# Kernel optimization log

Measured on AMD Instinct MI355X. Metric: run time of the kernel, lower is better.

Reference implementation:

```python
import jax, jax.numpy as jnp
import numpy as np

HIDDEN, HEADS, KV_HEADS, HEAD_DIM = 2048, 8, 1, 256
B, L = 2, 4096
ROPE_BASE = 10000.0


def _rope_tables(seq_len, dim, offset=0):
    inv_freq = 1.0 / (ROPE_BASE ** (jnp.arange(0, dim, 2, dtype=jnp.float32) / dim))
    t = jnp.arange(offset, offset + seq_len, dtype=jnp.float32)
    freqs = jnp.einsum('l,d->ld', t, inv_freq)          # [L, dim/2]
    emb = jnp.concatenate([freqs, freqs], axis=-1)      # [L, dim]
    return jnp.cos(emb), jnp.sin(emb)


def _rotate_half(x):
    x1, x2 = jnp.split(x, 2, axis=-1)
    return jnp.concatenate([-x2, x1], axis=-1)


def _apply_rope(x, cos, sin):
    # x: [B, H, L, D]; cos/sin: [L, D] broadcast over B, H
    return x * cos + _rotate_half(x) * sin


def setup_inputs() -> dict:
    key = jax.random.key(0)
    ks = jax.random.split(key, 5)
    s = lambda fan_in: 1.0 / np.sqrt(fan_in)
    return {
        'x':   jax.random.normal(ks[0], (B, L, HIDDEN), jnp.float32),
        'q_w': jax.random.normal(ks[1], (HEADS * HEAD_DIM, HIDDEN), jnp.float32) * s(HIDDEN),
        'k_w': jax.random.normal(ks[2], (KV_HEADS * HEAD_DIM, HIDDEN), jnp.float32) * s(HIDDEN),
        'v_w': jax.random.normal(ks[3], (KV_HEADS * HEAD_DIM, HIDDEN), jnp.float32) * s(HIDDEN),
        'o_w': jax.random.normal(ks[4], (HIDDEN, HEADS * HEAD_DIM), jnp.float32) * s(HEADS * HEAD_DIM),
    }


def reference(x, q_w, k_w, v_w, o_w):
    b, l, _ = x.shape
    g = HEADS // KV_HEADS  # kv groups
    # projections (nn.Linear: x @ W^T)
    q = (x @ q_w.T).reshape(b, l, HEADS, HEAD_DIM).transpose(0, 2, 1, 3)      # [B,H,L,D]
    k = (x @ k_w.T).reshape(b, l, KV_HEADS, HEAD_DIM).transpose(0, 2, 1, 3)   # [B,Hk,L,D]
    v = (x @ v_w.T).reshape(b, l, KV_HEADS, HEAD_DIM).transpose(0, 2, 1, 3)
    cos, sin = _rope_tables(l, HEAD_DIM, offset=0)
    q = _apply_rope(q, cos, sin)
    k = _apply_rope(k, cos, sin)
    # GQA attention without materializing repeated KV heads
    qg = q.reshape(b, KV_HEADS, g, l, HEAD_DIM)
    scale = HEAD_DIM ** -0.5
    scores = jnp.einsum('bkgqd,bkld->bkgql', qg, k) * scale                   # [B,Hk,g,L,L]
    attn = jax.nn.softmax(scores.astype(jnp.float32), axis=-1).astype(q.dtype)
    out = jnp.einsum('bkgql,bkld->bkgqd', attn, v)                            # [B,Hk,g,L,D]
    out = out.reshape(b, HEADS, l, HEAD_DIM).transpose(0, 2, 1, 3).reshape(b, l, HEADS * HEAD_DIM)
    return out @ o_w.T
```

## Files before the change

kernel.cpp:

```cpp
#include <hip/hip_runtime.h>
#include <cstdint>

typedef __bf16 bf16x8 __attribute__((ext_vector_type(8)));
typedef float f32x4 __attribute__((ext_vector_type(4)));
typedef float f32x16 __attribute__((ext_vector_type(16)));
typedef short s16x4 __attribute__((ext_vector_type(4)));
typedef int i32x4 __attribute__((ext_vector_type(4)));

static __device__ __forceinline__ short bf_bits(float f) {
  uint32_t u = __builtin_bit_cast(uint32_t, f);
  u += 0x7fffu + ((u >> 16) & 1u);
  return (short)(u >> 16);
}
static __device__ __forceinline__ float bf_f(short s) {
  uint32_t u = ((uint32_t)(uint16_t)s) << 16;
  return __builtin_bit_cast(float, u);
}
static __device__ __forceinline__ bf16x8 ld_frag(const short* p) {
  i32x4 v = *reinterpret_cast<const i32x4*>(p);
  return __builtin_bit_cast(bf16x8, v);
}

typedef __attribute__((address_space(3))) uint32_t lds_u32_t;
typedef const __attribute__((address_space(1))) uint32_t glb_u32_t;
static __device__ __forceinline__ void gl_lds16(const void* g, const void* l) {
  __builtin_amdgcn_global_load_lds((glb_u32_t*)g,
                                   (lds_u32_t*)(uint32_t)(uintptr_t)l,
                                   16, 0, 0);
}

__global__ void cvt_bf16(const float* __restrict__ in, short* __restrict__ out, int n4) {
  int i = blockIdx.x * blockDim.x + threadIdx.x;
  if (i >= n4) return;
  float4 v = reinterpret_cast<const float4*>(in)[i];
  s16x4 o = { bf_bits(v.x), bf_bits(v.y), bf_bits(v.z), bf_bits(v.w) };
  reinterpret_cast<s16x4*>(out)[i] = o;
}

__global__ void rope_table(float* __restrict__ ct, float* __restrict__ st) {
  int i = blockIdx.x * 256 + threadIdx.x;
  int l = i >> 7, d = i & 127;
  float inv = expf(-0.07195578415625f * (float)d);
  float f = (float)l * inv;
  ct[i] = cosf(f);
  st[i] = sinf(f);
}

__global__ void rope_apply(short* __restrict__ buf, const float* __restrict__ ct,
                           const float* __restrict__ st, int cbase, int hbits,
                           float scale, int total) {
  int i = blockIdx.x * blockDim.x + threadIdx.x;
  if (i >= total) return;
  int dg = i & 31;
  int h = (i >> 5) & ((1 << hbits) - 1);
  int tok = i >> (5 + hbits);
  int l = tok & 4095;
  long base = (long)tok * 2560 + cbase + h * 256;
  int d = dg * 4;
  s16x4 x1 = *reinterpret_cast<const s16x4*>(buf + base + d);
  s16x4 x2 = *reinterpret_cast<const s16x4*>(buf + base + d + 128);
  float4 c = *reinterpret_cast<const float4*>(ct + l * 128 + d);
  float4 s = *reinterpret_cast<const float4*>(st + l * 128 + d);
  s16x4 o1, o2;
  o1.x = bf_bits((bf_f(x1.x) * c.x - bf_f(x2.x) * s.x) * scale);
  o1.y = bf_bits((bf_f(x1.y) * c.y - bf_f(x2.y) * s.y) * scale);
  o1.z = bf_bits((bf_f(x1.z) * c.z - bf_f(x2.z) * s.z) * scale);
  o1.w = bf_bits((bf_f(x1.w) * c.w - bf_f(x2.w) * s.w) * scale);
  o2.x = bf_bits((bf_f(x2.x) * c.x + bf_f(x1.x) * s.x) * scale);
  o2.y = bf_bits((bf_f(x2.y) * c.y + bf_f(x1.y) * s.y) * scale);
  o2.z = bf_bits((bf_f(x2.z) * c.z + bf_f(x1.z) * s.z) * scale);
  o2.w = bf_bits((bf_f(x2.w) * c.w + bf_f(x1.w) * s.w) * scale);
  *reinterpret_cast<s16x4*>(buf + base + d) = o1;
  *reinterpret_cast<s16x4*>(buf + base + d + 128) = o2;
}

__global__ void transpose_v(const short* __restrict__ qkv, short* __restrict__ vt) {
  int i = blockIdx.x * 256 + threadIdx.x;
  int d = i & 255;
  int lg = (i >> 8) & 511;
  int b = i >> 17;
  const short* src = qkv + ((long)b * 4096 + lg * 8) * 2560 + 2304 + d;
  short tmp[8];
  #pragma unroll
  for (int j = 0; j < 8; ++j) tmp[j] = src[(long)j * 2560];
  short* dst = vt + ((long)b * 256 + d) * 4096 + lg * 8;
  s16x4 lo = { tmp[0], tmp[1], tmp[2], tmp[3] };
  s16x4 hi4 = { tmp[4], tmp[5], tmp[6], tmp[7] };
  *reinterpret_cast<s16x4*>(dst) = lo;
  *reinterpret_cast<s16x4*>(dst + 4) = hi4;
}

template <bool OUT_F32>
__global__ __launch_bounds__(256) void gemm_bt(const short* __restrict__ A,
                                               const short* __restrict__ B,
                                               void* __restrict__ C,
                                               int K, int ldc) {
  __shared__ short As[128 * 32];
  __shared__ short Bs[128 * 32];
  const int t = threadIdx.x;
  const int lane = t & 63;
  const int w = t >> 6;
  const long m0 = (long)blockIdx.x * 128;
  const long n0 = (long)blockIdx.y * 128;
  const int wr = (w >> 1) * 64, wc = (w & 1) * 64;
  const int fr = lane & 15, fk = (lane >> 4) * 8;
  f32x4 acc[4][4] = {};

  for (int k0 = 0; k0 < K; k0 += 32) {
    #pragma unroll
    for (int p = 0; p < 2; ++p) {
      int idx = p * 256 + t;
      gl_lds16(A + (m0 + (idx >> 2)) * K + k0 + (idx & 3) * 8, As + idx * 8);
    }
    #pragma unroll
    for (int p = 0; p < 2; ++p) {
      int idx = p * 256 + t;
      gl_lds16(B + (n0 + (idx >> 2)) * K + k0 + (idx & 3) * 8, Bs + idx * 8);
    }
    __syncthreads();
    bf16x8 af[4], bfr[4];
    #pragma unroll
    for (int i = 0; i < 4; ++i) af[i] = ld_frag(As + (wr + i * 16 + fr) * 32 + fk);
    #pragma unroll
    for (int j = 0; j < 4; ++j) bfr[j] = ld_frag(Bs + (wc + j * 16 + fr) * 32 + fk);
    #pragma unroll
    for (int i = 0; i < 4; ++i)
      #pragma unroll
      for (int j = 0; j < 4; ++j)
        acc[i][j] = __builtin_amdgcn_mfma_f32_16x16x32_bf16(af[i], bfr[j], acc[i][j], 0, 0, 0);
    __syncthreads();
  }
  const int er = lane >> 4, ec = lane & 15;
  #pragma unroll
  for (int i = 0; i < 4; ++i)
    #pragma unroll
    for (int j = 0; j < 4; ++j) {
      long col = n0 + wc + j * 16 + ec;
      #pragma unroll
      for (int r = 0; r < 4; ++r) {
        long row = m0 + wr + i * 16 + er * 4 + r;
        if constexpr (OUT_F32)
          reinterpret_cast<float*>(C)[row * ldc + col] = acc[i][j][r];
        else
          reinterpret_cast<short*>(C)[row * ldc + col] = bf_bits(acc[i][j][r]);
      }
    }
}

__global__ __launch_bounds__(256, 2) void attn(const short* __restrict__ qkv,
                                               const short* __restrict__ vtg,
                                               short* __restrict__ og) {
  __shared__ __align__(16) short KtS[2 * 32 * 256];
  __shared__ __align__(16) short VtS[2 * 256 * 32];
  const int t = threadIdx.x;
  const int lane = t & 63, w = t >> 6;
  const int lq = lane & 31, hi = lane >> 5;
  const int u = blockIdx.x;
  const int b = (u >> 2) & 1;
  const int local = (u & 3) | ((u >> 3) << 2);
  const int h = local >> 5;
  const int q0 = (local & 31) * 128;

  bf16x8 Qf[16];
  {
    const short* qp = qkv + ((long)(b * 4096 + q0 + w * 32 + lq)) * 2560 + h * 256;
    #pragma unroll
    for (int ds = 0; ds < 16; ++ds) Qf[ds] = ld_frag(qp + ds * 16 + hi * 8);
  }

  const short* kptr[4];
  const short* vptr[4];
  #pragma unroll
  for (int p = 0; p < 4; ++p) {
    int c = p * 256 + t;
    int r = c >> 5, s = c & 31;
    kptr[p] = qkv + ((long)(b * 4096 + r)) * 2560 + 2048 + ((s ^ (r & 7)) * 8);
  }
  #pragma unroll
  for (int p = 0; p < 4; ++p) {
    int c = p * 256 + t;
    int d = c >> 2, s = c & 3;
    vptr[p] = vtg + ((long)(b * 256 + d)) * 4096 + ((s ^ ((d >> 1) & 3)) * 8);
  }

#define STAGE(BUF) do {                                                          \
    _Pragma("unroll")                                                            \
    for (int p = 0; p < 4; ++p)                                                  \
      gl_lds16(kptr[p], KtS + (BUF) * 8192 + (p * 256 + t) * 8);                 \
    _Pragma("unroll")                                                            \
    for (int p = 0; p < 4; ++p)                                                  \
      gl_lds16(vptr[p], VtS + (BUF) * 8192 + (p * 256 + t) * 8);                 \
    _Pragma("unroll")                                                            \
    for (int p = 0; p < 4; ++p) { kptr[p] += 32 * 2560; vptr[p] += 32; }         \
  } while (0)

  STAGE(0);
  __syncthreads();

  f32x16 Oa[8] = {};
  float mrun = -3.0e38f, lrun = 0.0f;
  const int xk8 = (lq & 7) * 8;
  const int xv8 = ((lq >> 1) & 3) * 8;
  const int lv32 = lq * 32;
  int cur = 0;

  for (int kv0 = 0; kv0 < 4096; kv0 += 32) {
    if (kv0 + 32 < 4096) STAGE(cur ^ 1);
    const short* Kc = KtS + cur * 8192;
    const short* Vc = VtS + cur * 8192;

    f32x16 S = {};
    #pragma unroll
    for (int ds = 0; ds < 16; ++ds) {
      bf16x8 a = ld_frag(Kc + lq * 256 + ((ds * 16 + hi * 8) ^ xk8));
      S = __builtin_amdgcn_mfma_f32_32x32x16_bf16(a, Qf[ds], S, 0, 0, 0);
    }
    float smax = S[0];
    #pragma unroll
    for (int r = 1; r < 16; ++r) smax = fmaxf(smax, S[r]);
    smax = fmaxf(smax, __shfl_xor(smax, 32));

    if (__any(smax > mrun + 8.0f)) {
      float mnew = fmaxf(mrun, smax);
      float alpha = __expf(mrun - mnew);
      #pragma unroll
      for (int r = 0; r < 16; ++r) {
        int qp2 = (r & 3) + 8 * (r >> 2) + 4 * hi;
        float ar = __shfl(alpha, qp2);
        #pragma unroll
        for (int df = 0; df < 8; ++df) Oa[df][r] *= ar;
      }
      lrun *= alpha;
      mrun = mnew;
    }
    float psum = 0.0f;
    #pragma unroll
    for (int r = 0; r < 16; ++r) { S[r] = __expf(S[r] - mrun); psum += S[r]; }
    psum += __shfl_xor(psum, 32);
    lrun += psum;

    bf16x8 pa[2];
    #pragma unroll
    for (int kvs = 0; kvs < 2; ++kvs) {
      uint32_t x0, x1, y0, y1;
      asm("v_cvt_pk_bf16_f32 %0, %1, %2" : "=v"(x0) : "v"(S[8 * kvs + 0]), "v"(S[8 * kvs + 1]));
      asm("v_cvt_pk_bf16_f32 %0, %1, %2" : "=v"(x1) : "v"(S[8 * kvs + 2]), "v"(S[8 * kvs + 3]));
      asm("v_cvt_pk_bf16_f32 %0, %1, %2" : "=v"(y0) : "v"(S[8 * kvs + 4]), "v"(S[8 * kvs + 5]));
      asm("v_cvt_pk_bf16_f32 %0, %1, %2" : "=v"(y1) : "v"(S[8 * kvs + 6]), "v"(S[8 * kvs + 7]));
      asm("v_permlane32_swap_b32 %0, %1" : "+v"(x0), "+v"(y0));
      asm("v_permlane32_swap_b32 %0, %1" : "+v"(x1), "+v"(y1));
      i32x4 wv = { (int)x0, (int)x1, (int)y0, (int)y1 };
      pa[kvs] = __builtin_bit_cast(bf16x8, wv);
    }

    #pragma unroll
    for (int df = 0; df < 8; ++df)
      #pragma unroll
      for (int kvs = 0; kvs < 2; ++kvs) {
        bf16x8 vb = ld_frag(Vc + df * 1024 + lv32 + ((kvs * 16 + hi * 8) ^ xv8));
        Oa[df] = __builtin_amdgcn_mfma_f32_32x32x16_bf16(pa[kvs], vb, Oa[df], 0, 0, 0);
      }

    __syncthreads();
    cur ^= 1;
  }
#undef STAGE

  float linv = 1.0f / lrun;
  float lir[16];
  #pragma unroll
  for (int r = 0; r < 16; ++r) {
    int qp2 = (r & 3) + 8 * (r >> 2) + 4 * hi;
    lir[r] = __shfl(linv, qp2);
  }
  short* ob = og + ((long)(b * 4096 + q0)) * 2048 + h * 256;
  short* chunk = KtS;
  #pragma unroll
  for (int half = 0; half < 2; ++half) {
    __syncthreads();
    #pragma unroll
    for (int df4 = 0; df4 < 4; ++df4) {
      #pragma unroll
      for (int r = 0; r < 16; ++r) {
        int qp2 = (r & 3) + 8 * (r >> 2) + 4 * hi;
        chunk[(w * 32 + qp2) * 128 + df4 * 32 + lq] = bf_bits(Oa[half * 4 + df4][r] * lir[r]);
      }
    }
    __syncthreads();
    #pragma unroll
    for (int p = 0; p < 8; ++p) {
      int idx = p * 256 + t, row = idx >> 4, dg = idx & 15;
      i32x4 val = *reinterpret_cast<const i32x4*>(chunk + row * 128 + dg * 8);
      *reinterpret_cast<i32x4*>(ob + (long)row * 2048 + half * 128 + dg * 8) = val;
    }
  }
}

extern "C" void kernel_launch(void* const* d_in, const int* in_sizes, int n_in,
                              void* d_out, int out_size, void* d_ws, size_t ws_size,
                              hipStream_t stream) {
  const float* x  = (const float*)d_in[0];
  const float* qw = (const float*)d_in[1];
  const float* kw = (const float*)d_in[2];
  const float* vw = (const float*)d_in[3];
  const float* ow = (const float*)d_in[4];
  float* out = (float*)d_out;
  char* ws = (char*)d_ws;

  short* xb  = (short*)(ws);
  short* wb  = (short*)(ws + 33554432);
  short* qkv = (short*)(ws + 44040192);
  short* vtb = (short*)(ws + 85983232);
  float* ct  = (float*)(ws + 90177536);
  float* st  = (float*)(ws + 92274688);
  short* wob = (short*)(ws + 94371840);

  cvt_bf16<<<16384, 256, 0, stream>>>(x,  xb, 4194304);
  cvt_bf16<<<4096,  256, 0, stream>>>(qw, wb, 1048576);
  cvt_bf16<<<512,   256, 0, stream>>>(kw, wb + 2048 * 2048, 131072);
  cvt_bf16<<<512,   256, 0, stream>>>(vw, wb + 2304 * 2048, 131072);
  cvt_bf16<<<4096,  256, 0, stream>>>(ow, wob, 1048576);
  rope_table<<<2048, 256, 0, stream>>>(ct, st);

  gemm_bt<false><<<dim3(64, 20), 256, 0, stream>>>(xb, wb, qkv, 2048, 2560);

  rope_apply<<<8192, 256, 0, stream>>>(qkv, ct, st, 0,    3, 0.0625f, 2097152);
  rope_apply<<<1024, 256, 0, stream>>>(qkv, ct, st, 2048, 0, 1.0f,    262144);
  transpose_v<<<1024, 256, 0, stream>>>(qkv, vtb);

  attn<<<512, 256, 0, stream>>>(qkv, vtb, xb);

  gemm_bt<true><<<dim3(64, 16), 256, 0, stream>>>(xb, wob, out, 2048, 2048);
}
```

Measured before the change: 639.1 us.

## Register-staged KV prefetch, split QK accumulators, setprio, and XCD-aware GEMM tile swizzle

Replaces the direct global-to-LDS async copies for K/V tiles with loads into registers at the top of each iteration, followed by LDS stores after the PV MFMAs. This lets global latency overlap with compute and uses wider per-thread contiguous K reads. QK^T is split into two independent accumulator chains, and the max and sum reductions become trees, to shorten dependency chains. s_setprio is raised around the MFMA blocks. The projection GEMM remaps block indices so consecutive tiles are spread across the 8 XCDs. The register staging raises VGPR pressure, which could cut occupancy.

```diff
diff --git a/kernel.cpp b/kernel.cpp
--- a/kernel.cpp
+++ b/kernel.cpp
@@ -100,8 +100,11 @@
   const int t = threadIdx.x;
   const int lane = t & 63;
   const int w = t >> 6;
-  const long m0 = (long)blockIdx.x * 128;
-  const long n0 = (long)blockIdx.y * 128;
+  const int lin = blockIdx.x + gridDim.x * blockIdx.y;
+  const int cpx = (gridDim.x * gridDim.y) >> 3;
+  const int wrk = (lin & 7) * cpx + (lin >> 3);
+  const long m0 = (long)(wrk % gridDim.x) * 128;
+  const long n0 = (long)(wrk / gridDim.x) * 128;
   const int wr = (w >> 1) * 64, wc = (w & 1) * 64;
   const int fr = lane & 15, fk = (lane >> 4) * 8;
   f32x4 acc[4][4] = {};
@@ -168,33 +171,29 @@
     for (int ds = 0; ds < 16; ++ds) Qf[ds] = ld_frag(qp + ds * 16 + hi * 8);
   }
 
-  const short* kptr[4];
-  const short* vptr[4];
-  #pragma unroll
-  for (int p = 0; p < 4; ++p) {
-    int c = p * 256 + t;
-    int r = c >> 5, s = c & 31;
-    kptr[p] = qkv + ((long)(b * 4096 + r)) * 2560 + 2048 + ((s ^ (r & 7)) * 8);
-  }
-  #pragma unroll
-  for (int p = 0; p < 4; ++p) {
-    int c = p * 256 + t;
-    int d = c >> 2, s = c & 3;
-    vptr[p] = vtg + ((long)(b * 256 + d)) * 4096 + ((s ^ ((d >> 1) & 3)) * 8);
-  }
-
-#define STAGE(BUF) do {                                                          \
-    _Pragma("unroll")                                                            \
-    for (int p = 0; p < 4; ++p)                                                  \
-      gl_lds16(kptr[p], KtS + (BUF) * 8192 + (p * 256 + t) * 8);                 \
-    _Pragma("unroll")                                                            \
-    for (int p = 0; p < 4; ++p)                                                  \
-      gl_lds16(vptr[p], VtS + (BUF) * 8192 + (p * 256 + t) * 8);                 \
-    _Pragma("unroll")                                                            \
-    for (int p = 0; p < 4; ++p) { kptr[p] += 32 * 2560; vptr[p] += 32; }         \
-  } while (0)
-
-  STAGE(0);
+  const int kr = t & 31, kq = t >> 5;
+  const int vsl = t & 3, vd0 = t >> 2;
+  const short* kg0 = qkv + ((long)(b * 4096 + kr)) * 2560 + 2048 + kq * 32;
+  const short* vg0 = vtg + ((long)(b * 256 + vd0)) * 4096 + vsl * 8;
+  int kwo[4], vwo[4];
+  #pragma unroll
+  for (int c = 0; c < 4; ++c) {
+    kwo[c] = kr * 256 + (((kq * 4 + c) ^ (kr & 7)) * 8);
+    int d = vd0 + 64 * c;
+    vwo[c] = d * 32 + ((vsl ^ ((d >> 1) & 3)) * 8);
+  }
+
+  {
+    i32x4 kreg[4], vreg[4];
+    #pragma unroll
+    for (int c = 0; c < 4; ++c) kreg[c] = *reinterpret_cast<const i32x4*>(kg0 + c * 8);
+    #pragma unroll
+    for (int c = 0; c < 4; ++c) vreg[c] = *reinterpret_cast<const i32x4*>(vg0 + (long)c * 64 * 4096);
+    #pragma unroll
+    for (int c = 0; c < 4; ++c) *reinterpret_cast<i32x4*>(KtS + kwo[c]) = kreg[c];
+    #pragma unroll
+    for (int c = 0; c < 4; ++c) *reinterpret_cast<i32x4*>(VtS + vwo[c]) = vreg[c];
+  }
   __syncthreads();
 
   f32x16 Oa[8] = {};
@@ -205,19 +204,38 @@
   int cur = 0;
 
   for (int kv0 = 0; kv0 < 4096; kv0 += 32) {
-    if (kv0 + 32 < 4096) STAGE(cur ^ 1);
+    i32x4 kreg[4], vreg[4];
+    const bool pf = (kv0 + 32) < 4096;
+    if (pf) {
+      const short* kp = kg0 + (long)(kv0 + 32) * 2560;
+      const short* vp = vg0 + kv0 + 32;
+      #pragma unroll
+      for (int c = 0; c < 4; ++c) kreg[c] = *reinterpret_cast<const i32x4*>(kp + c * 8);
+      #pragma unroll
+      for (int c = 0; c < 4; ++c) vreg[c] = *reinterpret_cast<const i32x4*>(vp + (long)c * 64 * 4096);
+    }
     const short* Kc = KtS + cur * 8192;
     const short* Vc = VtS + cur * 8192;
 
-    f32x16 S = {};
-    #pragma unroll
-    for (int ds = 0; ds < 16; ++ds) {
-      bf16x8 a = ld_frag(Kc + lq * 256 + ((ds * 16 + hi * 8) ^ xk8));
-      S = __builtin_amdgcn_mfma_f32_32x32x16_bf16(a, Qf[ds], S, 0, 0, 0);
-    }
-    float smax = S[0];
-    #pragma unroll
-    for (int r = 1; r < 16; ++r) smax = fmaxf(smax, S[r]);
+    f32x16 S0 = {}, S1 = {};
+    __builtin_amdgcn_s_setprio(1);
+    #pragma unroll
+    for (int ds = 0; ds < 8; ++ds) {
+      bf16x8 a0 = ld_frag(Kc + lq * 256 + ((ds * 16 + hi * 8) ^ xk8));
+      bf16x8 a1 = ld_frag(Kc + lq * 256 + (((ds + 8) * 16 + hi * 8) ^ xk8));
+      S0 = __builtin_amdgcn_mfma_f32_32x32x16_bf16(a0, Qf[ds], S0, 0, 0, 0);
+      S1 = __builtin_amdgcn_mfma_f32_32x32x16_bf16(a1, Qf[ds + 8], S1, 0, 0, 0);
+    }
+    __builtin_amdgcn_s_setprio(0);
+    f32x16 S;
+    #pragma unroll
+    for (int r = 0; r < 16; ++r) S[r] = S0[r] + S1[r];
+
+    float t8[8];
+    #pragma unroll
+    for (int r = 0; r < 8; ++r) t8[r] = fmaxf(S[r], S[r + 8]);
+    float smax = fmaxf(fmaxf(fmaxf(t8[0], t8[4]), fmaxf(t8[1], t8[5])),
+                       fmaxf(fmaxf(t8[2], t8[6]), fmaxf(t8[3], t8[7])));
     smax = fmaxf(smax, __shfl_xor(smax, 32));
 
     if (__any(smax > mrun + 8.0f)) {
@@ -233,9 +251,12 @@
       lrun *= alpha;
       mrun = mnew;
     }
-    float psum = 0.0f;
-    #pragma unroll
-    for (int r = 0; r < 16; ++r) { S[r] = __expf(S[r] - mrun); psum += S[r]; }
+    #pragma unroll
+    for (int r = 0; r < 16; ++r) S[r] = __expf(S[r] - mrun);
+    float p8[8];
+    #pragma unroll
+    for (int r = 0; r < 8; ++r) p8[r] = S[r] + S[r + 8];
+    float psum = (p8[0] + p8[4]) + (p8[1] + p8[5]) + ((p8[2] + p8[6]) + (p8[3] + p8[7]));
     psum += __shfl_xor(psum, 32);
     lrun += psum;
 
@@ -253,6 +274,7 @@
       pa[kvs] = __builtin_bit_cast(bf16x8, wv);
     }
 
+    __builtin_amdgcn_s_setprio(1);
     #pragma unroll
     for (int df = 0; df < 8; ++df)
       #pragma unroll
@@ -260,11 +282,17 @@
         bf16x8 vb = ld_frag(Vc + df * 1024 + lv32 + ((kvs * 16 + hi * 8) ^ xv8));
         Oa[df] = __builtin_amdgcn_mfma_f32_32x32x16_bf16(pa[kvs], vb, Oa[df], 0, 0, 0);
       }
-
+    __builtin_amdgcn_s_setprio(0);
+
+    if (pf) {
+      #pragma unroll
+      for (int c = 0; c < 4; ++c) *reinterpret_cast<i32x4*>(KtS + (cur ^ 1) * 8192 + kwo[c]) = kreg[c];
+      #pragma unroll
+      for (int c = 0; c < 4; ++c) *reinterpret_cast<i32x4*>(VtS + (cur ^ 1) * 8192 + vwo[c]) = vreg[c];
+    }
     __syncthreads();
     cur ^= 1;
   }
-#undef STAGE
 
   float linv = 1.0f / lrun;
   float lir[16];
```

Result: slower. 1.011 ms (+58.2%).
